# Performance work log

Measured on AMD Instinct MI355X. Metric: run time of the kernel, lower is better.

## Reference

```python
import jax, jax.numpy as jnp
import numpy as np
import math

ALPHA_MIN = math.exp(-1.0 / 5.0)   # ~0.8187
ALPHA_MAX = math.exp(-1.0 / 25.0)  # ~0.9608
THRESHOLD = 1.0


def setup_inputs() -> dict:
    key = jax.random.key(0)
    k1, k2, k3, k4, k5 = jax.random.split(key, 5)
    B, T, I, H = 32, 2048, 256, 512
    x = jax.random.normal(k1, (B, T, I), dtype=jnp.float32)
    # Linear weight, kaiming-ish scale
    W = jax.random.normal(k2, (H, I), dtype=jnp.float32) * (1.0 / np.sqrt(I))
    # alpha ~ U[exp(-1/5), exp(-1/25)] as in nn.init.uniform_
    alpha = ALPHA_MIN + jax.random.uniform(k3, (H,), dtype=jnp.float32) * (ALPHA_MAX - ALPHA_MIN)
    # initial membrane potential / spike state (torch.rand in _lif_cell)
    u0 = jax.random.uniform(k4, (B, H), dtype=jnp.float32)
    s0 = jax.random.uniform(k5, (B, H), dtype=jnp.float32)
    return {"x": x, "W": W, "alpha": alpha, "u0": u0, "s0": s0}


def reference(x, W, alpha, u0, s0):
    # clamp alpha to its admissible range (lif_feature has no 'NoClamp')
    alpha = jnp.clip(alpha, ALPHA_MIN, ALPHA_MAX)
    b = 1.0 - alpha  # lif_feature has no 'B'

    # feedforward projection: [B, T, H]
    Wx = jnp.einsum('bti,hi->bth', x, W)

    def step(carry, wx_t):
        ut, st = carry
        ut = alpha * (ut - st) + b * wx_t          # leaky integrate + soft reset
        st = (ut - THRESHOLD > 0).astype(ut.dtype)  # heaviside spike
        return (ut, st), st

    # scan over time: Wx -> [T, B, H]
    _, s = jax.lax.scan(step, (u0, s0), jnp.swapaxes(Wx, 0, 1))
    return jnp.swapaxes(s, 0, 1)  # [B, T, H]
```

## Files before the change

kernel.cpp:

```cpp
#include <hip/hip_runtime.h>

#define ALPHA_MIN 0.8187307530779818f
#define ALPHA_MAX 0.9607894391523232f

typedef _Float16 f16;
typedef _Float16 f16x4 __attribute__((ext_vector_type(4)));
typedef _Float16 f16x8 __attribute__((ext_vector_type(8)));
typedef float f32x16 __attribute__((ext_vector_type(16)));

#define BB_ 32
#define TT_ 2048
#define KK_ 256
#define HH_ 512
#define TC_ 64
#define KH_ 128
#define CPB_ 16

__device__ __forceinline__ void barrier_lds() {
    __builtin_amdgcn_s_waitcnt(0xC07F);
    __builtin_amdgcn_s_barrier();
}

__global__ __launch_bounds__(512, 1) void wx_gemm(
    const float* __restrict__ X,
    const float* __restrict__ W,
    float* __restrict__ out)
{
    __shared__ f16 Ah[2][TC_ * KH_];
    __shared__ f16 Al[2][TC_ * KH_];

    const int b    = blockIdx.x & 31;
    const int nt   = (blockIdx.x >> 5) & 7;
    const int half = blockIdx.x >> 8;
    const int n0   = nt * 64;
    const int c0   = half * CPB_;
    const int c1   = c0 + CPB_;

    const int tid  = threadIdx.x;
    const int wv   = tid >> 6;
    const int lane = tid & 63;
    const int fm   = lane & 31;
    const int fq   = lane >> 5;

    if (wv < 4) {
        const int mh = wv >> 1;
        const int nh = wv & 1;

        f16x8 bh[16], bl[16];
        {
            const float* wp = W + (size_t)(n0 + nh * 32 + fm) * KK_ + fq * 8;
#pragma unroll
            for (int ks = 0; ks < 16; ++ks) {
                float4 v0 = *(const float4*)(wp + ks * 16);
                float4 v1 = *(const float4*)(wp + ks * 16 + 4);
                float v[8] = {v0.x, v0.y, v0.z, v0.w, v1.x, v1.y, v1.z, v1.w};
                f16x8 h, l;
#pragma unroll
                for (int j = 0; j < 8; ++j) {
                    const f16 hj = (f16)v[j];
                    h[j] = hj;
                    l[j] = (f16)((v[j] - (float)hj) * 2048.0f);
                }
                bh[ks] = h; bl[ks] = l;
            }
        }

        f32x16 accH, accLa, accLb;
#pragma unroll
        for (int e = 0; e < 16; ++e) { accH[e] = 0.0f; accLa[e] = 0.0f; accLb[e] = 0.0f; }

        const int row = mh * 32 + fm;
        const int r15 = row & 15;

        auto compute_half = [&](int hf) {
            __builtin_amdgcn_s_setprio(1);
#pragma unroll
            for (int ks = 0; ks < 8; ++ks) {
                const int addr = row * KH_ + (((ks * 2 + fq) ^ r15) * 8);
                const f16x8 ah = *(const f16x8*)&Ah[hf][addr];
                const f16x8 al = *(const f16x8*)&Al[hf][addr];
                const int ksg = hf * 8 + ks;
                accH  = __builtin_amdgcn_mfma_f32_32x32x16_f16(ah, bh[ksg], accH,  0, 0, 0);
                accLa = __builtin_amdgcn_mfma_f32_32x32x16_f16(ah, bl[ksg], accLa, 0, 0, 0);
                accLb = __builtin_amdgcn_mfma_f32_32x32x16_f16(al, bh[ksg], accLb, 0, 0, 0);
            }
            __builtin_amdgcn_s_setprio(0);
        };

        barrier_lds();
        for (int c = c0; c < c1; ++c) {
            compute_half(0);
            barrier_lds();
            compute_half(1);
            {
                float* op = out + ((size_t)b * TT_ + (size_t)c * TC_) * HH_ + n0;
                const int colw = nh * 32 + fm;
#pragma unroll
                for (int r = 0; r < 16; ++r) {
                    const int roww = mh * 32 + (r & 3) + 8 * (r >> 2) + 4 * fq;
                    op[(size_t)roww * HH_ + colw] =
                        accH[r] + (accLa[r] + accLb[r]) * (1.0f / 2048.0f);
                    accH[r] = 0.0f; accLa[r] = 0.0f; accLb[r] = 0.0f;
                }
            }
            barrier_lds();
        }
    } else {
        const int u      = wv - 4;
        const int srow_j = u * 16 + (lane >> 5);
        const int f4i    = lane & 31;
        const int g      = f4i >> 1;
        const int sub    = f4i & 1;

        float4 pA[8], pB[8];

        auto issueA = [&](int hs) {
            const int c = hs >> 1, kh = hs & 1;
            const float* base = X + ((size_t)b * TT_ + (size_t)c * TC_) * KK_ + kh * KH_ + f4i * 4;
#pragma unroll
            for (int j = 0; j < 8; ++j)
                pA[j] = *(const float4*)(base + (size_t)(srow_j + j * 2) * KK_);
        };
        auto issueB = [&](int hs) {
            const int c = hs >> 1, kh = hs & 1;
            const float* base = X + ((size_t)b * TT_ + (size_t)c * TC_) * KK_ + kh * KH_ + f4i * 4;
#pragma unroll
            for (int j = 0; j < 8; ++j)
                pB[j] = *(const float4*)(base + (size_t)(srow_j + j * 2) * KK_);
        };
        auto cvtA = [&](int bufi) {
#pragma unroll
            for (int j = 0; j < 8; ++j) {
                const int rowa = srow_j + j * 2;
                const float v[4] = {pA[j].x, pA[j].y, pA[j].z, pA[j].w};
                f16x4 h, l;
#pragma unroll
                for (int e = 0; e < 4; ++e) {
                    const f16 he = (f16)v[e];
                    h[e] = he;
                    l[e] = (f16)((v[e] - (float)he) * 2048.0f);
                }
                const int addr = rowa * KH_ + ((g ^ (rowa & 15)) * 8) + sub * 4;
                *(f16x4*)&Ah[bufi][addr] = h;
                *(f16x4*)&Al[bufi][addr] = l;
            }
        };
        auto cvtB = [&](int bufi) {
#pragma unroll
            for (int j = 0; j < 8; ++j) {
                const int rowa = srow_j + j * 2;
                const float v[4] = {pB[j].x, pB[j].y, pB[j].z, pB[j].w};
                f16x4 h, l;
#pragma unroll
                for (int e = 0; e < 4; ++e) {
                    const f16 he = (f16)v[e];
                    h[e] = he;
                    l[e] = (f16)((v[e] - (float)he) * 2048.0f);
                }
                const int addr = rowa * KH_ + ((g ^ (rowa & 15)) * 8) + sub * 4;
                *(f16x4*)&Ah[bufi][addr] = h;
                *(f16x4*)&Al[bufi][addr] = l;
            }
        };

        issueA(2 * c0);
        issueB(2 * c0 + 1);
        cvtA(0);
        issueA(2 * c0 + 2);
        barrier_lds();

        for (int c = c0; c < c1; ++c) {
            cvtB(1);
            if (c + 1 < c1) issueB(2 * c + 3);
            barrier_lds();
            if (c + 1 < c1) cvtA(0);
            if (c + 2 < c1) issueA(2 * c + 4);
            barrier_lds();
        }
    }
}

__global__ __launch_bounds__(64) void lif_scan_opt(
    float* __restrict__ buf,
    const float* __restrict__ alpha,
    const float* __restrict__ u0,
    const float* __restrict__ s0)
{
    const int chain = blockIdx.x * 64 + threadIdx.x;
    const int h = chain & (HH_ - 1);
    const int b = chain >> 9;
    float a = alpha[h];
    a = fminf(fmaxf(a, ALPHA_MIN), ALPHA_MAX);
    const float bbv = 1.0f - a;
    float u = u0[chain];
    float s = s0[chain];
    float* base = buf + (size_t)b * TT_ * HH_ + h;

    float wA[32], wB[32];

    auto loadA = [&](int t0) {
#pragma unroll
        for (int i = 0; i < 32; ++i) wA[i] = base[(size_t)(t0 + i) * HH_];
    };
    auto loadB = [&](int t0) {
#pragma unroll
        for (int i = 0; i < 32; ++i) wB[i] = base[(size_t)(t0 + i) * HH_];
    };
    auto stepA = [&](int t0) {
#pragma unroll
        for (int i = 0; i < 32; ++i) {
            u = fmaf(a, u - s, bbv * wA[i]);
            s = (u > 1.0f) ? 1.0f : 0.0f;
            base[(size_t)(t0 + i) * HH_] = s;
        }
    };
    auto stepB = [&](int t0) {
#pragma unroll
        for (int i = 0; i < 32; ++i) {
            u = fmaf(a, u - s, bbv * wB[i]);
            s = (u > 1.0f) ? 1.0f : 0.0f;
            base[(size_t)(t0 + i) * HH_] = s;
        }
    };

    loadA(0);
    for (int t0 = 0; t0 < TT_; t0 += 64) {
        loadB(t0 + 32);
        stepA(t0);
        if (t0 + 64 < TT_) loadA(t0 + 64);
        stepB(t0 + 32);
    }
}

__global__ void gemm_naive(const float* __restrict__ X, const float* __restrict__ W,
                           float* __restrict__ C, int M, int N, int K)
{
    const int idx = blockIdx.x * 256 + threadIdx.x;
    if (idx >= M * N) return;
    const int m = idx / N, n = idx % N;
    float acc = 0.0f;
    for (int k = 0; k < K; ++k) acc = fmaf(X[(size_t)m * K + k], W[(size_t)n * K + k], acc);
    C[idx] = acc;
}

__global__ __launch_bounds__(64) void lif_scan_inplace(
    float* __restrict__ buf, const float* __restrict__ alpha,
    const float* __restrict__ u0, const float* __restrict__ s0, int T, int H)
{
    const int chain = blockIdx.x * 64 + threadIdx.x;
    const int h = chain % H;
    const int b = chain / H;
    float a = alpha[h];
    a = fminf(fmaxf(a, ALPHA_MIN), ALPHA_MAX);
    const float bb = 1.0f - a;
    float u = u0[chain], s = s0[chain];
    float* base = buf + (size_t)b * T * H + h;
    for (int t = 0; t < T; ++t) {
        u = fmaf(a, u - s, bb * base[(size_t)t * H]);
        s = (u > 1.0f) ? 1.0f : 0.0f;
        base[(size_t)t * H] = s;
    }
}

extern "C" void kernel_launch(void* const* d_in, const int* in_sizes, int n_in,
                              void* d_out, int out_size, void* d_ws, size_t ws_size,
                              hipStream_t stream) {
    const float* x     = (const float*)d_in[0];
    const float* W     = (const float*)d_in[1];
    const float* alpha = (const float*)d_in[2];
    const float* u0    = (const float*)d_in[3];
    const float* s0    = (const float*)d_in[4];
    float* out = (float*)d_out;

    const int H = in_sizes[2];
    const int I = in_sizes[1] / H;
    const int B = in_sizes[3] / H;
    const int T = in_sizes[0] / (B * I);

    if (B == BB_ && T == TT_ && I == KK_ && H == HH_) {
        wx_gemm<<<512, 512, 0, stream>>>(x, W, out);
        lif_scan_opt<<<256, 64, 0, stream>>>(out, alpha, u0, s0);
    } else {
        const int M = B * T;
        gemm_naive<<<(M * H + 255) / 256, 256, 0, stream>>>(x, W, out, M, H, I);
        lif_scan_inplace<<<(B * H + 63) / 64, 64, 0, stream>>>(out, alpha, u0, s0, T, H);
    }
}
```

Baseline: 301.6 us.

## Write GEMM output to blocked workspace and scan with 512-thread blocks

The GEMM can now write Wx into a workspace in a blocked layout ([b][ntile][t][64]), so each 64-column tile is stored contiguously over time. A new scan kernel uses one 512-thread block per batch row. Each wave reads contiguous 256-byte rows from the workspace and writes spikes to the output. The aim is better read locality, but this adds a separate workspace write and read instead of updating in place. The scan launches only 32 blocks, which may underfill the GPU compared with the previous 256 small blocks.

```diff
diff --git a/kernel.cpp b/kernel.cpp
--- a/kernel.cpp
+++ b/kernel.cpp
@@ -21,10 +21,11 @@
     __builtin_amdgcn_s_barrier();
 }
 
+template <bool BLOCKED>
 __global__ __launch_bounds__(512, 1) void wx_gemm(
     const float* __restrict__ X,
     const float* __restrict__ W,
-    float* __restrict__ out)
+    float* __restrict__ dst)
 {
     __shared__ f16 Ah[2][TC_ * KH_];
     __shared__ f16 Al[2][TC_ * KH_];
@@ -93,12 +94,20 @@
             barrier_lds();
             compute_half(1);
             {
-                float* op = out + ((size_t)b * TT_ + (size_t)c * TC_) * HH_ + n0;
                 const int colw = nh * 32 + fm;
+                float* op;
+                size_t rstride;
+                if (BLOCKED) {
+                    op = dst + ((size_t)(b * 8 + nt) * TT_ + (size_t)c * TC_) * 64;
+                    rstride = 64;
+                } else {
+                    op = dst + ((size_t)b * TT_ + (size_t)c * TC_) * HH_ + n0;
+                    rstride = HH_;
+                }
 #pragma unroll
                 for (int r = 0; r < 16; ++r) {
                     const int roww = mh * 32 + (r & 3) + 8 * (r >> 2) + 4 * fq;
-                    op[(size_t)roww * HH_ + colw] =
+                    op[(size_t)roww * rstride + colw] =
                         accH[r] + (accLa[r] + accLb[r]) * (1.0f / 2048.0f);
                     accH[r] = 0.0f; accLa[r] = 0.0f; accLb[r] = 0.0f;
                 }
@@ -177,6 +186,63 @@
             if (c + 2 < c1) issueA(2 * c + 4);
             barrier_lds();
         }
+    }
+}
+
+__global__ __launch_bounds__(512, 1) void lif_scan32(
+    const float* __restrict__ ws,
+    float* __restrict__ out,
+    const float* __restrict__ alpha,
+    const float* __restrict__ u0,
+    const float* __restrict__ s0)
+{
+    const int b  = blockIdx.x;
+    const int h  = threadIdx.x;
+    const int nt = h >> 6;
+    const float* wsrc = ws + (size_t)(b * 8 + nt) * TT_ * 64 + (h & 63);
+    float* op = out + (size_t)b * TT_ * HH_ + h;
+
+    const int chain = b * HH_ + h;
+    float a = alpha[h];
+    a = fminf(fmaxf(a, ALPHA_MIN), ALPHA_MAX);
+    const float bbv = 1.0f - a;
+    float u = u0[chain];
+    float s = s0[chain];
+
+    float wA[32], wB[32];
+
+    auto loadA = [&](int t0) {
+#pragma unroll
+        for (int i = 0; i < 32; ++i) wA[i] = wsrc[(size_t)(t0 + i) * 64];
+    };
+    auto loadB = [&](int t0) {
+#pragma unroll
+        for (int i = 0; i < 32; ++i) wB[i] = wsrc[(size_t)(t0 + i) * 64];
+    };
+    auto stepA = [&](int t0) {
+#pragma unroll
+        for (int i = 0; i < 32; ++i) {
+            u = fmaf(a, u - s, bbv * wA[i]);
+            s = (u > 1.0f) ? 1.0f : 0.0f;
+            op[(size_t)(t0 + i) * HH_] = s;
+        }
+    };
+    auto stepB = [&](int t0) {
+#pragma unroll
+        for (int i = 0; i < 32; ++i) {
+            u = fmaf(a, u - s, bbv * wB[i]);
+            s = (u > 1.0f) ? 1.0f : 0.0f;
+            op[(size_t)(t0 + i) * HH_] = s;
+        }
+    };
+
+    loadA(0);
+    for (int t0 = 0; t0 < TT_; t0 += 64) {
+        loadB(t0 + 32);
+        stepA(t0);
+        if (t0 + 64 < TT_) loadA(t0 + 64);
+        stepB(t0 + 32);
+        __syncthreads();
     }
 }
 
@@ -197,7 +263,6 @@
     float* base = buf + (size_t)b * TT_ * HH_ + h;
 
     float wA[32], wB[32];
-
     auto loadA = [&](int t0) {
 #pragma unroll
         for (int i = 0; i < 32; ++i) wA[i] = base[(size_t)(t0 + i) * HH_];
@@ -278,8 +343,15 @@
     const int T = in_sizes[0] / (B * I);
 
     if (B == BB_ && T == TT_ && I == KK_ && H == HH_) {
-        wx_gemm<<<512, 512, 0, stream>>>(x, W, out);
-        lif_scan_opt<<<256, 64, 0, stream>>>(out, alpha, u0, s0);
+        const size_t wx_bytes = (size_t)BB_ * TT_ * HH_ * sizeof(float);
+        if (ws_size >= wx_bytes) {
+            float* wx = (float*)d_ws;
+            wx_gemm<true><<<512, 512, 0, stream>>>(x, W, wx);
+            lif_scan32<<<32, 512, 0, stream>>>(wx, out, alpha, u0, s0);
+        } else {
+            wx_gemm<false><<<512, 512, 0, stream>>>(x, W, out);
+            lif_scan_opt<<<256, 64, 0, stream>>>(out, alpha, u0, s0);
+        }
     } else {
         const int M = B * T;
         gemm_naive<<<(M * H + 255) / 256, 256, 0, stream>>>(x, W, out, M, H, I);
```

After: 372.7 us. 1.24x slower.

## Replace LDS-staged warp-specialized GEMM with direct-from-global register GEMM

Applied to the files above, without the earlier changes.

Drops the producer/consumer wave split and the LDS double buffer in the Wx projection. Each wave now loads its own X rows straight from global memory into registers, splits them into hi/lo fp16 and feeds the MFMAs, with a three-deep register prefetch. The grid grows to 2048 blocks of 256 threads, so more blocks can be resident and there are no barriers. The cost is that X tiles are loaded redundantly across the four waves of a block and the four H-groups, and latency hiding now relies on the cache and on occupancy.

```diff
diff --git a/kernel.cpp b/kernel.cpp
--- a/kernel.cpp
+++ b/kernel.cpp
@@ -4,7 +4,6 @@
 #define ALPHA_MAX 0.9607894391523232f
 
 typedef _Float16 f16;
-typedef _Float16 f16x4 __attribute__((ext_vector_type(4)));
 typedef _Float16 f16x8 __attribute__((ext_vector_type(8)));
 typedef float f32x16 __attribute__((ext_vector_type(16)));
 
@@ -12,29 +11,16 @@
 #define TT_ 2048
 #define KK_ 256
 #define HH_ 512
-#define TC_ 64
-#define KH_ 128
-#define CPB_ 16
-
-__device__ __forceinline__ void barrier_lds() {
-    __builtin_amdgcn_s_waitcnt(0xC07F);
-    __builtin_amdgcn_s_barrier();
-}
-
-__global__ __launch_bounds__(512, 1) void wx_gemm(
+
+__global__ __launch_bounds__(256) void wx_gemm_nolds(
     const float* __restrict__ X,
     const float* __restrict__ W,
     float* __restrict__ out)
 {
-    __shared__ f16 Ah[2][TC_ * KH_];
-    __shared__ f16 Al[2][TC_ * KH_];
-
-    const int b    = blockIdx.x & 31;
-    const int nt   = (blockIdx.x >> 5) & 7;
-    const int half = blockIdx.x >> 8;
-    const int n0   = nt * 64;
-    const int c0   = half * CPB_;
-    const int c1   = c0 + CPB_;
+    const int bid = blockIdx.x;
+    const int hg  = bid & 3;
+    const int tc  = (bid >> 2) & 15;
+    const int b   = bid >> 6;
 
     const int tid  = threadIdx.x;
     const int wv   = tid >> 6;
@@ -42,140 +28,70 @@
     const int fm   = lane & 31;
     const int fq   = lane >> 5;
 
-    if (wv < 4) {
-        const int mh = wv >> 1;
-        const int nh = wv & 1;
-
-        f16x8 bh[16], bl[16];
-        {
-            const float* wp = W + (size_t)(n0 + nh * 32 + fm) * KK_ + fq * 8;
-#pragma unroll
-            for (int ks = 0; ks < 16; ++ks) {
-                float4 v0 = *(const float4*)(wp + ks * 16);
-                float4 v1 = *(const float4*)(wp + ks * 16 + 4);
-                float v[8] = {v0.x, v0.y, v0.z, v0.w, v1.x, v1.y, v1.z, v1.w};
-                f16x8 h, l;
-#pragma unroll
-                for (int j = 0; j < 8; ++j) {
-                    const f16 hj = (f16)v[j];
-                    h[j] = hj;
-                    l[j] = (f16)((v[j] - (float)hj) * 2048.0f);
-                }
-                bh[ks] = h; bl[ks] = l;
+    const int h0 = hg * 128 + wv * 32;
+
+    f16x8 bh[16], bl[16];
+    {
+        const float* wp = W + (size_t)(h0 + fm) * KK_ + fq * 8;
+#pragma unroll
+        for (int ks = 0; ks < 16; ++ks) {
+            float4 v0 = *(const float4*)(wp + ks * 16);
+            float4 v1 = *(const float4*)(wp + ks * 16 + 4);
+            float v[8] = {v0.x, v0.y, v0.z, v0.w, v1.x, v1.y, v1.z, v1.w};
+            f16x8 h, l;
+#pragma unroll
+            for (int j = 0; j < 8; ++j) {
+                const f16 hj = (f16)v[j];
+                h[j] = hj;
+                l[j] = (f16)((v[j] - (float)hj) * 2048.0f);
             }
-        }
+            bh[ks] = h; bl[ks] = l;
+        }
+    }
+
+    const float* xtile = X + ((size_t)b * TT_ + (size_t)tc * 128) * KK_;
+
+#pragma unroll 1
+    for (int sub = 0; sub < 4; ++sub) {
+        const float* xrow = xtile + (size_t)(sub * 32 + fm) * KK_ + fq * 8;
 
         f32x16 accH, accLa, accLb;
 #pragma unroll
         for (int e = 0; e < 16; ++e) { accH[e] = 0.0f; accLa[e] = 0.0f; accLb[e] = 0.0f; }
 
-        const int row = mh * 32 + fm;
-        const int r15 = row & 15;
-
-        auto compute_half = [&](int hf) {
-            __builtin_amdgcn_s_setprio(1);
-#pragma unroll
-            for (int ks = 0; ks < 8; ++ks) {
-                const int addr = row * KH_ + (((ks * 2 + fq) ^ r15) * 8);
-                const f16x8 ah = *(const f16x8*)&Ah[hf][addr];
-                const f16x8 al = *(const f16x8*)&Al[hf][addr];
-                const int ksg = hf * 8 + ks;
-                accH  = __builtin_amdgcn_mfma_f32_32x32x16_f16(ah, bh[ksg], accH,  0, 0, 0);
-                accLa = __builtin_amdgcn_mfma_f32_32x32x16_f16(ah, bl[ksg], accLa, 0, 0, 0);
-                accLb = __builtin_amdgcn_mfma_f32_32x32x16_f16(al, bh[ksg], accLb, 0, 0, 0);
+        float4 p[3][2];
+        p[0][0] = *(const float4*)(xrow + 0 * 16);
+        p[0][1] = *(const float4*)(xrow + 0 * 16 + 4);
+        p[1][0] = *(const float4*)(xrow + 1 * 16);
+        p[1][1] = *(const float4*)(xrow + 1 * 16 + 4);
+
+#pragma unroll
+        for (int ks = 0; ks < 16; ++ks) {
+            if (ks + 2 < 16) {
+                p[(ks + 2) % 3][0] = *(const float4*)(xrow + (ks + 2) * 16);
+                p[(ks + 2) % 3][1] = *(const float4*)(xrow + (ks + 2) * 16 + 4);
             }
-            __builtin_amdgcn_s_setprio(0);
-        };
-
-        barrier_lds();
-        for (int c = c0; c < c1; ++c) {
-            compute_half(0);
-            barrier_lds();
-            compute_half(1);
-            {
-                float* op = out + ((size_t)b * TT_ + (size_t)c * TC_) * HH_ + n0;
-                const int colw = nh * 32 + fm;
-#pragma unroll
-                for (int r = 0; r < 16; ++r) {
-                    const int roww = mh * 32 + (r & 3) + 8 * (r >> 2) + 4 * fq;
-                    op[(size_t)roww * HH_ + colw] =
-                        accH[r] + (accLa[r] + accLb[r]) * (1.0f / 2048.0f);
-                    accH[r] = 0.0f; accLa[r] = 0.0f; accLb[r] = 0.0f;
-                }
+            const float4 v0 = p[ks % 3][0];
+            const float4 v1 = p[ks % 3][1];
+            const float v[8] = {v0.x, v0.y, v0.z, v0.w, v1.x, v1.y, v1.z, v1.w};
+            f16x8 ah, al;
+#pragma unroll
+            for (int j = 0; j < 8; ++j) {
+                const f16 hj = (f16)v[j];
+                ah[j] = hj;
+                al[j] = (f16)((v[j] - (float)hj) * 2048.0f);
             }
-            barrier_lds();
-        }
-    } else {
-        const int u      = wv - 4;
-        const int srow_j = u * 16 + (lane >> 5);
-        const int f4i    = lane & 31;
-        const int g      = f4i >> 1;
-        const int sub    = f4i & 1;
-
-        float4 pA[8], pB[8];
-
-        auto issueA = [&](int hs) {
-            const int c = hs >> 1, kh = hs & 1;
-            const float* base = X + ((size_t)b * TT_ + (size_t)c * TC_) * KK_ + kh * KH_ + f4i * 4;
-#pragma unroll
-            for (int j = 0; j < 8; ++j)
-                pA[j] = *(const float4*)(base + (size_t)(srow_j + j * 2) * KK_);
-        };
-        auto issueB = [&](int hs) {
-            const int c = hs >> 1, kh = hs & 1;
-            const float* base = X + ((size_t)b * TT_ + (size_t)c * TC_) * KK_ + kh * KH_ + f4i * 4;
-#pragma unroll
-            for (int j = 0; j < 8; ++j)
-                pB[j] = *(const float4*)(base + (size_t)(srow_j + j * 2) * KK_);
-        };
-        auto cvtA = [&](int bufi) {
-#pragma unroll
-            for (int j = 0; j < 8; ++j) {
-                const int rowa = srow_j + j * 2;
-                const float v[4] = {pA[j].x, pA[j].y, pA[j].z, pA[j].w};
-                f16x4 h, l;
-#pragma unroll
-                for (int e = 0; e < 4; ++e) {
-                    const f16 he = (f16)v[e];
-                    h[e] = he;
-                    l[e] = (f16)((v[e] - (float)he) * 2048.0f);
-                }
-                const int addr = rowa * KH_ + ((g ^ (rowa & 15)) * 8) + sub * 4;
-                *(f16x4*)&Ah[bufi][addr] = h;
-                *(f16x4*)&Al[bufi][addr] = l;
-            }
-        };
-        auto cvtB = [&](int bufi) {
-#pragma unroll
-            for (int j = 0; j < 8; ++j) {
-                const int rowa = srow_j + j * 2;
-                const float v[4] = {pB[j].x, pB[j].y, pB[j].z, pB[j].w};
-                f16x4 h, l;
-#pragma unroll
-                for (int e = 0; e < 4; ++e) {
-                    const f16 he = (f16)v[e];
-                    h[e] = he;
-                    l[e] = (f16)((v[e] - (float)he) * 2048.0f);
-                }
-                const int addr = rowa * KH_ + ((g ^ (rowa & 15)) * 8) + sub * 4;
-                *(f16x4*)&Ah[bufi][addr] = h;
-                *(f16x4*)&Al[bufi][addr] = l;
-            }
-        };
-
-        issueA(2 * c0);
-        issueB(2 * c0 + 1);
-        cvtA(0);
-        issueA(2 * c0 + 2);
-        barrier_lds();
-
-        for (int c = c0; c < c1; ++c) {
-            cvtB(1);
-            if (c + 1 < c1) issueB(2 * c + 3);
-            barrier_lds();
-            if (c + 1 < c1) cvtA(0);
-            if (c + 2 < c1) issueA(2 * c + 4);
-            barrier_lds();
+            accH  = __builtin_amdgcn_mfma_f32_32x32x16_f16(ah, bh[ks], accH,  0, 0, 0);
+            accLa = __builtin_amdgcn_mfma_f32_32x32x16_f16(ah, bl[ks], accLa, 0, 0, 0);
+            accLb = __builtin_amdgcn_mfma_f32_32x32x16_f16(al, bh[ks], accLb, 0, 0, 0);
+        }
+
+        float* op = out + ((size_t)b * TT_ + (size_t)tc * 128 + sub * 32) * HH_ + h0;
+#pragma unroll
+        for (int r = 0; r < 16; ++r) {
+            const int roww = (r & 3) + 8 * (r >> 2) + 4 * fq;
+            op[(size_t)roww * HH_ + fm] =
+                accH[r] + (accLa[r] + accLb[r]) * (1.0f / 2048.0f);
         }
     }
 }
@@ -197,7 +113,6 @@
     float* base = buf + (size_t)b * TT_ * HH_ + h;
 
     float wA[32], wB[32];
-
     auto loadA = [&](int t0) {
 #pragma unroll
         for (int i = 0; i < 32; ++i) wA[i] = base[(size_t)(t0 + i) * HH_];
@@ -278,7 +193,7 @@
     const int T = in_sizes[0] / (B * I);
 
     if (B == BB_ && T == TT_ && I == KK_ && H == HH_) {
-        wx_gemm<<<512, 512, 0, stream>>>(x, W, out);
+        wx_gemm_nolds<<<2048, 256, 0, stream>>>(x, W, out);
         lif_scan_opt<<<256, 64, 0, stream>>>(out, alpha, u0, s0);
     } else {
         const int M = B * T;
```

Measured after the change: 400.1 us. 32.7% more time.

## Shrink GEMM time tile and split time into more blocks

Applied to the files above, without the earlier changes.

Halves the time-chunk size of the Wx GEMM tile to 32 rows, uses 256-thread blocks (2 MFMA waves and 2 loader waves), and splits the time axis into 8 segments, launching 2048 blocks instead of 512. This adds parallelism so more CUs stay busy and LDS use per block drops, which may allow several blocks per CU. In exchange each block reloads and reconverts its W fragments into registers, and each compute wave issues fewer MFMAs per barrier.

```diff
diff --git a/kernel.cpp b/kernel.cpp
--- a/kernel.cpp
+++ b/kernel.cpp
@@ -12,16 +12,16 @@
 #define TT_ 2048
 #define KK_ 256
 #define HH_ 512
-#define TC_ 64
+#define TC_ 32
 #define KH_ 128
-#define CPB_ 16
+#define CPS_ 8
 
 __device__ __forceinline__ void barrier_lds() {
     __builtin_amdgcn_s_waitcnt(0xC07F);
     __builtin_amdgcn_s_barrier();
 }
 
-__global__ __launch_bounds__(512, 1) void wx_gemm(
+__global__ __launch_bounds__(256, 1) void wx_gemm32(
     const float* __restrict__ X,
     const float* __restrict__ W,
     float* __restrict__ out)
@@ -31,10 +31,9 @@
 
     const int b    = blockIdx.x & 31;
     const int nt   = (blockIdx.x >> 5) & 7;
-    const int half = blockIdx.x >> 8;
+    const int tseg = blockIdx.x >> 8;
     const int n0   = nt * 64;
-    const int c0   = half * CPB_;
-    const int c1   = c0 + CPB_;
+    const int trow0 = tseg * (CPS_ * TC_);
 
     const int tid  = threadIdx.x;
     const int wv   = tid >> 6;
@@ -42,9 +41,8 @@
     const int fm   = lane & 31;
     const int fq   = lane >> 5;
 
-    if (wv < 4) {
-        const int mh = wv >> 1;
-        const int nh = wv & 1;
+    if (wv < 2) {
+        const int nh = wv;
 
         f16x8 bh[16], bl[16];
         {
@@ -69,7 +67,7 @@
 #pragma unroll
         for (int e = 0; e < 16; ++e) { accH[e] = 0.0f; accLa[e] = 0.0f; accLb[e] = 0.0f; }
 
-        const int row = mh * 32 + fm;
+        const int row = fm;
         const int r15 = row & 15;
 
         auto compute_half = [&](int hf) {
@@ -88,16 +86,16 @@
         };
 
         barrier_lds();
-        for (int c = c0; c < c1; ++c) {
+        for (int c = 0; c < CPS_; ++c) {
             compute_half(0);
             barrier_lds();
             compute_half(1);
             {
-                float* op = out + ((size_t)b * TT_ + (size_t)c * TC_) * HH_ + n0;
+                float* op = out + ((size_t)b * TT_ + trow0 + c * TC_) * HH_ + n0;
                 const int colw = nh * 32 + fm;
 #pragma unroll
                 for (int r = 0; r < 16; ++r) {
-                    const int roww = mh * 32 + (r & 3) + 8 * (r >> 2) + 4 * fq;
+                    const int roww = (r & 3) + 8 * (r >> 2) + 4 * fq;
                     op[(size_t)roww * HH_ + colw] =
                         accH[r] + (accLa[r] + accLb[r]) * (1.0f / 2048.0f);
                     accH[r] = 0.0f; accLa[r] = 0.0f; accLb[r] = 0.0f;
@@ -106,7 +104,7 @@
             barrier_lds();
         }
     } else {
-        const int u      = wv - 4;
+        const int u      = wv - 2;
         const int srow_j = u * 16 + (lane >> 5);
         const int f4i    = lane & 31;
         const int g      = f4i >> 1;
@@ -116,14 +114,16 @@
 
         auto issueA = [&](int hs) {
             const int c = hs >> 1, kh = hs & 1;
-            const float* base = X + ((size_t)b * TT_ + (size_t)c * TC_) * KK_ + kh * KH_ + f4i * 4;
+            const float* base = X + ((size_t)b * TT_ + trow0 + (size_t)c * TC_) * KK_
+                                  + kh * KH_ + f4i * 4;
 #pragma unroll
             for (int j = 0; j < 8; ++j)
                 pA[j] = *(const float4*)(base + (size_t)(srow_j + j * 2) * KK_);
         };
         auto issueB = [&](int hs) {
             const int c = hs >> 1, kh = hs & 1;
-            const float* base = X + ((size_t)b * TT_ + (size_t)c * TC_) * KK_ + kh * KH_ + f4i * 4;
+            const float* base = X + ((size_t)b * TT_ + trow0 + (size_t)c * TC_) * KK_
+                                  + kh * KH_ + f4i * 4;
 #pragma unroll
             for (int j = 0; j < 8; ++j)
                 pB[j] = *(const float4*)(base + (size_t)(srow_j + j * 2) * KK_);
@@ -163,18 +163,18 @@
             }
         };
 
-        issueA(2 * c0);
-        issueB(2 * c0 + 1);
+        issueA(0);
+        issueB(1);
         cvtA(0);
-        issueA(2 * c0 + 2);
+        issueA(2);
         barrier_lds();
 
-        for (int c = c0; c < c1; ++c) {
+        for (int c = 0; c < CPS_; ++c) {
             cvtB(1);
-            if (c + 1 < c1) issueB(2 * c + 3);
-            barrier_lds();
-            if (c + 1 < c1) cvtA(0);
-            if (c + 2 < c1) issueA(2 * c + 4);
+            if (c + 1 < CPS_) issueB(2 * c + 3);
+            barrier_lds();
+            if (c + 1 < CPS_) cvtA(0);
+            if (c + 2 < CPS_) issueA(2 * c + 4);
             barrier_lds();
         }
     }
@@ -197,7 +197,6 @@
     float* base = buf + (size_t)b * TT_ * HH_ + h;
 
     float wA[32], wB[32];
-
     auto loadA = [&](int t0) {
 #pragma unroll
         for (int i = 0; i < 32; ++i) wA[i] = base[(size_t)(t0 + i) * HH_];
@@ -278,7 +277,7 @@
     const int T = in_sizes[0] / (B * I);
 
     if (B == BB_ && T == TT_ && I == KK_ && H == HH_) {
-        wx_gemm<<<512, 512, 0, stream>>>(x, W, out);
+        wx_gemm32<<<2048, 256, 0, stream>>>(x, W, out);
         lif_scan_opt<<<256, 64, 0, stream>>>(out, alpha, u0, s0);
     } else {
         const int M = B * T;
```

Measured after the change: 317.3 us. 5.2% more time.
